# Optimization experiments

Measured on AMD Instinct MI355X. Metric: run time of the kernel, lower is better.

The kernel has to match this reference:

```python
import jax, jax.numpy as jnp
import numpy as np

B, T, D = 2048, 200, 64
H1, H2 = 80, 40
CONST_MIN = -4294967295.0


def setup_inputs() -> dict:
    key = jax.random.key(0)
    ks = jax.random.split(key, 10)
    q = jax.random.normal(ks[0], (B, D), dtype=jnp.float32)
    k = jax.random.normal(ks[1], (B, T, D), dtype=jnp.float32)
    v = jax.random.normal(ks[2], (B, T, D), dtype=jnp.float32)
    mask = jax.random.randint(ks[3], (B, T), 0, 2, dtype=jnp.int32)
    # MLP params: Dense(80, sigmoid) -> Dense(40, sigmoid) -> Dense(1)
    s1 = 1.0 / np.sqrt(4 * D)
    W1 = jax.random.normal(ks[4], (4 * D, H1), dtype=jnp.float32) * s1
    b1 = jnp.zeros((H1,), dtype=jnp.float32)
    W2 = jax.random.normal(ks[5], (H1, H2), dtype=jnp.float32) * (1.0 / np.sqrt(H1))
    b2 = jnp.zeros((H2,), dtype=jnp.float32)
    Wf = jax.random.normal(ks[6], (H2, 1), dtype=jnp.float32) * (1.0 / np.sqrt(H2))
    bf = jnp.zeros((1,), dtype=jnp.float32)
    return {"q": q, "k": k, "v": v, "mask": mask,
            "W1": W1, "b1": b1, "W2": W2, "b2": b2, "Wf": Wf, "bf": bf}


def reference(q, k, v, mask, W1, b1, W2, b2, Wf, bf):
    # q: [B,D] tiled over T -> [B,T,D]
    qt = jnp.broadcast_to(q[:, None, :], k.shape)
    # per-pair features [B,T,4D]
    info = jnp.concatenate([qt, k, qt - k, qt * k], axis=-1)
    h = jax.nn.sigmoid(jnp.einsum('btf,fh->bth', info, W1) + b1)
    h = jax.nn.sigmoid(jnp.einsum('bth,hg->btg', h, W2) + b2)
    logits = (jnp.einsum('btg,go->bto', h, Wf) + bf)[..., 0]  # [B,T]
    logits = jnp.where(mask == 0, jnp.float32(CONST_MIN), logits)
    w = jax.nn.softmax(logits, axis=-1)  # [B,T]
    out = jnp.einsum('bt,btd->bd', w, v)  # weighted sum of v
    return out
```

## Files before the change

kernel.cpp:

```cpp
#include <hip/hip_runtime.h>
#include <math.h>

#define T_LEN 200

typedef short bf8 __attribute__((ext_vector_type(8)));
typedef float f32x4 __attribute__((ext_vector_type(4)));

__device__ __forceinline__ float sigmoidf_(float x){ return 1.0f/(1.0f+__expf(-x)); }
__device__ __forceinline__ unsigned int pk_bf16(float lo, float hi){
  unsigned int r; asm("v_cvt_pk_bf16_f32 %0, %1, %2":"=v"(r):"v"(lo),"v"(hi)); return r;
}
__device__ __forceinline__ float bfu(short s){
  union{unsigned u; float f;} c; c.u = ((unsigned)(unsigned short)s)<<16; return c.f;
}
union U4B8 { uint4 u; bf8 b; };
__device__ __forceinline__ bf8 pack8(float4 x, float4 y){
  U4B8 r;
  r.u.x = pk_bf16(x.x,x.y); r.u.y = pk_bf16(x.z,x.w);
  r.u.z = pk_bf16(y.x,y.y); r.u.w = pk_bf16(y.z,y.w);
  return r.b;
}
__device__ __forceinline__ bf8 combine8(bf8 fbc, bf8 fd, float4 ql, float4 qh){
  U4B8 r;
  r.u.x = pk_bf16(fmaf(ql.x, bfu(fd[0]), bfu(fbc[0])), fmaf(ql.y, bfu(fd[1]), bfu(fbc[1])));
  r.u.y = pk_bf16(fmaf(ql.z, bfu(fd[2]), bfu(fbc[2])), fmaf(ql.w, bfu(fd[3]), bfu(fbc[3])));
  r.u.z = pk_bf16(fmaf(qh.x, bfu(fd[4]), bfu(fbc[4])), fmaf(qh.y, bfu(fd[5]), bfu(fbc[5])));
  r.u.w = pk_bf16(fmaf(qh.z, bfu(fd[6]), bfu(fbc[6])), fmaf(qh.w, bfu(fd[7]), bfu(fbc[7])));
  return r.b;
}

__global__ void prep_kernel(const float* __restrict__ W1, const float* __restrict__ W2,
                            const float* __restrict__ b2, const float* __restrict__ Wf,
                            float* __restrict__ wsf){
  unsigned short* fb = (unsigned short*)wsf;
  int i = blockIdx.x*256 + threadIdx.x;
  if (i < 15360){
    int fi = i >> 9;
    int lane = (i>>3)&63, e = i&7;
    int ht = fi/6, ks = fi%6;
    int h = ht*16 + (lane&15);
    int f = ks*32 + ((lane>>4)<<3) + e;
    float val;
    if (f < 64)        val = W1[(64+f)*80+h] - W1[(128+f)*80+h];
    else if (f < 128)  val = W1[(128+f)*80+h];
    else               val = W1[(f-128)*80+h] + W1[f*80+h];
    fb[i] = (unsigned short)(pk_bf16(val,val) & 0xffffu);
  }
  if (i < 4608){
    int fi = i >> 9;
    int lane = (i>>3)&63, e = i&7;
    int gt = fi/3, ks = fi%3;
    int g = gt*16 + (lane&15);
    int h = ks*32 + ((lane>>4)<<3) + e;
    float val;
    if (g < 40 && h < 80)       val = W2[h*40+g];
    else if (g < 40 && h == 80) val = b2[g];
    else                        val = 0.f;
    fb[15360+i] = (unsigned short)(pk_bf16(val,val) & 0xffffu);
  }
  if (i < 48){
    wsf[10032 + i] = (i<40) ? Wf[i] : 0.f;
  }
}

__global__ __launch_bounds__(64, 1) void fused_kernel(
    const float* __restrict__ q, const float* __restrict__ k, const float* __restrict__ v,
    const int* __restrict__ mask, const float* __restrict__ b1,
    const float* __restrict__ bf, const float* __restrict__ wsf,
    float* __restrict__ out)
{
  __shared__ unsigned short tl[224];
  __shared__ __align__(16) unsigned int Hw[2][16*52];
  __shared__ float e_lds[16];
  __shared__ __align__(16) unsigned int w2s[9*64*4];

  const int lane = threadIdx.x;
  const int lg = lane>>4, lc = lane&15;
  const long b = blockIdx.x;

  const float* kb = k + b*(T_LEN*64);
  const float* vb = v + b*(T_LEN*64);
  const int*   mb = mask + b*T_LEN;
  const float* qb = q + b*64;
  const unsigned short* fbg = (const unsigned short*)wsf;
  const bf8* A1f = (const bf8*)fbg;
  const uint4* A2u = (const uint4*)(fbg + 15360);
  const float* wfp = wsf + 10032;

  { uint4 z = {0,0,0,0};
    if (!(lane&1)) z.x = 0x00003F80u;
    *(uint4*)(&Hw[lane>>5][((lane&31)>>1)*52 + 40 + (lane&1)*4]) = z; }

  #pragma unroll
  for (int i=0;i<9;++i) ((uint4*)w2s)[i*64+lane] = A2u[i*64+lane];

  float4 qA0 = *(const float4*)(qb + lg*8);
  float4 qA1 = *(const float4*)(qb + lg*8 + 4);
  float4 qB0 = *(const float4*)(qb + 32 + lg*8);
  float4 qB1 = *(const float4*)(qb + 32 + lg*8 + 4);

  bf8 wk[10];
  #pragma unroll
  for (int ht=0; ht<5; ++ht){
    wk[ht*2+0] = combine8(A1f[(ht*6+0)*64+lane], A1f[(ht*6+2)*64+lane], qA0, qA1);
    wk[ht*2+1] = combine8(A1f[(ht*6+1)*64+lane], A1f[(ht*6+3)*64+lane], qB0, qB1);
  }
  float wfv[12];
  #pragma unroll
  for (int gt=0; gt<3; ++gt){
    float4 wv = *(const float4*)(wfp + gt*16 + lg*4);
    wfv[gt*4+0]=wv.x; wfv[gt*4+1]=wv.y; wfv[gt*4+2]=wv.z; wfv[gt*4+3]=wv.w;
  }

  f32x4 qacc[5];
  {
    bf8 fq0 = pack8(qA0,qA1);
    bf8 fq1 = pack8(qB0,qB1);
    #pragma unroll
    for (int ht=0; ht<5; ++ht){
      float4 bv = *(const float4*)(b1 + ht*16 + lg*4);
      qacc[ht][0]=bv.x; qacc[ht][1]=bv.y; qacc[ht][2]=bv.z; qacc[ht][3]=bv.w;
      qacc[ht] = __builtin_amdgcn_mfma_f32_16x16x32_bf16(A1f[(ht*6+4)*64+lane], fq0, qacc[ht],0,0,0);
      qacc[ht] = __builtin_amdgcn_mfma_f32_16x16x32_bf16(A1f[(ht*6+5)*64+lane], fq1, qacc[ht],0,0,0);
    }
  }
  const float bf0 = bf[0];

  int tot = 0;
  unsigned long long ltm = (1ull<<lane) - 1ull;
  #pragma unroll
  for (int c=0;c<4;++c){
    int t = c*64 + lane;
    bool f = (t < T_LEN) && (mb[t] != 0);
    unsigned long long bal = __ballot(f);
    if (f) tl[tot + (int)__popcll(bal & ltm)] = (unsigned short)t;
    tot += (int)__popcll(bal);
  }

  if (tot == 0){
    float accv = 0.f;
    for (int t=0; t<T_LEN; ++t) accv += vb[t*64 + lane];
    out[b*64 + lane] = accv * (1.0f/(float)T_LEN);
    return;
  }

  int tp = tl[min(lc, tot-1)];
  const float* kr = kb + tp*64 + lg*8;
  float4 na0 = *(const float4*)(kr);
  float4 na1 = *(const float4*)(kr+4);
  float4 nb0 = *(const float4*)(kr+32);
  float4 nb1 = *(const float4*)(kr+36);
  float vcur[16];
  #pragma unroll
  for (int i=0;i<16;++i){
    int ti = tl[min(i, tot-1)];
    vcur[i] = vb[ti*64 + lane];
  }

  float acc_pv0 = 0.f, acc_pv1 = 0.f;
  float se0 = 0.f, se1 = 0.f;
  int buf = 0;
  for (int base = 0; base < tot; base += 16, buf ^= 1){
    const bool have_next = (base + 16 < tot);
    bf8 f0 = pack8(na0,na1);
    bf8 f1 = pack8(nb0,nb1);
    float vnxt[16];
    if (have_next){
      int tn = tl[min(base+16+lc, tot-1)];
      const float* krn = kb + tn*64 + lg*8;
      na0 = *(const float4*)(krn);
      na1 = *(const float4*)(krn+4);
      nb0 = *(const float4*)(krn+32);
      nb1 = *(const float4*)(krn+36);
      #pragma unroll
      for (int i=0;i<16;++i){
        int ti = tl[min(base+16+i, tot-1)];
        vnxt[i] = vb[ti*64 + lane];
      }
    }

    f32x4 acc[5];
    #pragma unroll
    for (int ht=0; ht<5; ++ht) acc[ht] = qacc[ht];
    #pragma unroll
    for (int ht=0; ht<5; ++ht){
      acc[ht] = __builtin_amdgcn_mfma_f32_16x16x32_bf16(wk[ht*2+0], f0, acc[ht],0,0,0);
      acc[ht] = __builtin_amdgcn_mfma_f32_16x16x32_bf16(wk[ht*2+1], f1, acc[ht],0,0,0);
    }

    unsigned int* Hb = &Hw[buf][0];
    #pragma unroll
    for (int ht=0; ht<5; ++ht){
      #pragma unroll
      for (int rp=0; rp<2; ++rp)
        Hb[lc*52 + ht*8+lg*2+rp] = pk_bf16(sigmoidf_(acc[ht][2*rp]), sigmoidf_(acc[ht][2*rp+1]));
    }

    bf8 c0[3];
    #pragma unroll
    for (int ks=0; ks<3; ++ks) c0[ks] = *(const bf8*)(Hb + lc*52 + 16*ks + 4*lg);
    f32x4 g0[3];
    #pragma unroll
    for (int gt=0; gt<3; ++gt){ g0[gt][0]=0.f; g0[gt][1]=0.f; g0[gt][2]=0.f; g0[gt][3]=0.f; }
    #pragma unroll
    for (int gt=0; gt<3; ++gt){
      #pragma unroll
      for (int ks=0; ks<3; ++ks){
        bf8 wf2 = *(const bf8*)(w2s + ((gt*3+ks)*64+lane)*4);
        g0[gt] = __builtin_amdgcn_mfma_f32_16x16x32_bf16(wf2, c0[ks], g0[gt],0,0,0);
      }
    }
    float p0=0.f;
    #pragma unroll
    for (int gt=0; gt<3; ++gt){
      #pragma unroll
      for (int r=0;r<4;++r) p0 = fmaf(wfv[gt*4+r], sigmoidf_(g0[gt][r]), p0);
    }
    p0 += __shfl_xor(p0,16); p0 += __shfl_xor(p0,32);
    if (lg == 0) e_lds[lc] = (base+lc < tot) ? __expf(p0 + bf0) : 0.f;

    #pragma unroll
    for (int i=0;i<16;i+=2){
      float ei0 = e_lds[i];
      float ei1 = e_lds[i+1];
      se0 += ei0; se1 += ei1;
      acc_pv0 = fmaf(ei0, vcur[i],   acc_pv0);
      acc_pv1 = fmaf(ei1, vcur[i+1], acc_pv1);
    }
    if (have_next){
      #pragma unroll
      for (int i=0;i<16;++i) vcur[i] = vnxt[i];
    }
  }

  out[b*64 + lane] = (acc_pv0 + acc_pv1) / (se0 + se1);
}

extern "C" void kernel_launch(void* const* d_in, const int* in_sizes, int n_in,
                              void* d_out, int out_size, void* d_ws, size_t ws_size,
                              hipStream_t stream) {
  const float* q    = (const float*)d_in[0];
  const float* k    = (const float*)d_in[1];
  const float* v    = (const float*)d_in[2];
  const int*   mask = (const int*)d_in[3];
  const float* W1   = (const float*)d_in[4];
  const float* b1   = (const float*)d_in[5];
  const float* W2   = (const float*)d_in[6];
  const float* b2   = (const float*)d_in[7];
  const float* Wf   = (const float*)d_in[8];
  const float* bf   = (const float*)d_in[9];
  float* out = (float*)d_out;
  float* wsf = (float*)d_ws;

  hipLaunchKernelGGL(prep_kernel, dim3(60), dim3(256), 0, stream, W1, W2, b2, Wf, wsf);
  hipLaunchKernelGGL(fused_kernel, dim3(2048), dim3(64), 0, stream,
                     q, k, v, mask, b1, bf, wsf, out);
}
```

Measured before the change: 38.54 us.

## Process 32 keys per iteration with two interleaved MFMA chains

Widens the main loop from 16 to 32 unmasked positions per iteration. Two independent MFMA accumulator sets now interleave for both MLP layers, which adds instruction-level parallelism and halves the loop trips and barrier-like LDS round trips. The k prefetch is doubled, but v is now loaded at the top of each iteration instead of being prefetched a chunk ahead, so v load latency may be exposed. Register pressure also rises, and the single Hw buffer drops the previous double buffering.

```diff
diff --git a/kernel.cpp b/kernel.cpp
--- a/kernel.cpp
+++ b/kernel.cpp
@@ -70,8 +70,8 @@
     float* __restrict__ out)
 {
   __shared__ unsigned short tl[224];
-  __shared__ __align__(16) unsigned int Hw[2][16*52];
-  __shared__ float e_lds[16];
+  __shared__ __align__(16) unsigned int Hw[32*52];
+  __shared__ float e_lds[32];
   __shared__ __align__(16) unsigned int w2s[9*64*4];
 
   const int lane = threadIdx.x;
@@ -89,7 +89,7 @@
 
   { uint4 z = {0,0,0,0};
     if (!(lane&1)) z.x = 0x00003F80u;
-    *(uint4*)(&Hw[lane>>5][((lane&31)>>1)*52 + 40 + (lane&1)*4]) = z; }
+    *(uint4*)(&Hw[(lane>>1)*52 + 40 + (lane&1)*4]) = z; }
 
   #pragma unroll
   for (int i=0;i<9;++i) ((uint4*)w2s)[i*64+lane] = A2u[i*64+lane];
@@ -144,92 +144,112 @@
     return;
   }
 
-  int tp = tl[min(lc, tot-1)];
-  const float* kr = kb + tp*64 + lg*8;
-  float4 na0 = *(const float4*)(kr);
-  float4 na1 = *(const float4*)(kr+4);
-  float4 nb0 = *(const float4*)(kr+32);
-  float4 nb1 = *(const float4*)(kr+36);
-  float vcur[16];
-  #pragma unroll
-  for (int i=0;i<16;++i){
-    int ti = tl[min(i, tot-1)];
-    vcur[i] = vb[ti*64 + lane];
-  }
+  int t0 = tl[min(lc, tot-1)];
+  int t1 = tl[min(16+lc, tot-1)];
+  const float* kr0 = kb + t0*64 + lg*8;
+  const float* kr1 = kb + t1*64 + lg*8;
+  float4 ka0 = *(const float4*)(kr0);
+  float4 ka1 = *(const float4*)(kr0+4);
+  float4 kb0 = *(const float4*)(kr0+32);
+  float4 kb1 = *(const float4*)(kr0+36);
+  float4 kc0 = *(const float4*)(kr1);
+  float4 kc1 = *(const float4*)(kr1+4);
+  float4 kd0 = *(const float4*)(kr1+32);
+  float4 kd1 = *(const float4*)(kr1+36);
 
   float acc_pv0 = 0.f, acc_pv1 = 0.f;
   float se0 = 0.f, se1 = 0.f;
-  int buf = 0;
-  for (int base = 0; base < tot; base += 16, buf ^= 1){
-    const bool have_next = (base + 16 < tot);
-    bf8 f0 = pack8(na0,na1);
-    bf8 f1 = pack8(nb0,nb1);
-    float vnxt[16];
+  for (int base = 0; base < tot; base += 32){
+    const bool have_next = (base + 32 < tot);
+    bf8 f0 = pack8(ka0,ka1);
+    bf8 f1 = pack8(kb0,kb1);
+    bf8 f2 = pack8(kc0,kc1);
+    bf8 f3 = pack8(kd0,kd1);
+    float vcur[32];
+    #pragma unroll
+    for (int i=0;i<32;++i){
+      int ti = tl[min(base+i, tot-1)];
+      vcur[i] = vb[ti*64 + lane];
+    }
     if (have_next){
-      int tn = tl[min(base+16+lc, tot-1)];
-      const float* krn = kb + tn*64 + lg*8;
-      na0 = *(const float4*)(krn);
-      na1 = *(const float4*)(krn+4);
-      nb0 = *(const float4*)(krn+32);
-      nb1 = *(const float4*)(krn+36);
-      #pragma unroll
-      for (int i=0;i<16;++i){
-        int ti = tl[min(base+16+i, tot-1)];
-        vnxt[i] = vb[ti*64 + lane];
-      }
-    }
-
-    f32x4 acc[5];
-    #pragma unroll
-    for (int ht=0; ht<5; ++ht) acc[ht] = qacc[ht];
+      int tn0 = tl[min(base+32+lc, tot-1)];
+      int tn1 = tl[min(base+48+lc, tot-1)];
+      const float* krn0 = kb + tn0*64 + lg*8;
+      const float* krn1 = kb + tn1*64 + lg*8;
+      ka0 = *(const float4*)(krn0);
+      ka1 = *(const float4*)(krn0+4);
+      kb0 = *(const float4*)(krn0+32);
+      kb1 = *(const float4*)(krn0+36);
+      kc0 = *(const float4*)(krn1);
+      kc1 = *(const float4*)(krn1+4);
+      kd0 = *(const float4*)(krn1+32);
+      kd1 = *(const float4*)(krn1+36);
+    }
+
+    f32x4 acc0[5], acc1[5];
+    #pragma unroll
+    for (int ht=0; ht<5; ++ht){ acc0[ht] = qacc[ht]; acc1[ht] = qacc[ht]; }
     #pragma unroll
     for (int ht=0; ht<5; ++ht){
-      acc[ht] = __builtin_amdgcn_mfma_f32_16x16x32_bf16(wk[ht*2+0], f0, acc[ht],0,0,0);
-      acc[ht] = __builtin_amdgcn_mfma_f32_16x16x32_bf16(wk[ht*2+1], f1, acc[ht],0,0,0);
-    }
-
-    unsigned int* Hb = &Hw[buf][0];
+      acc0[ht] = __builtin_amdgcn_mfma_f32_16x16x32_bf16(wk[ht*2+0], f0, acc0[ht],0,0,0);
+      acc0[ht] = __builtin_amdgcn_mfma_f32_16x16x32_bf16(wk[ht*2+1], f1, acc0[ht],0,0,0);
+      acc1[ht] = __builtin_amdgcn_mfma_f32_16x16x32_bf16(wk[ht*2+0], f2, acc1[ht],0,0,0);
+      acc1[ht] = __builtin_amdgcn_mfma_f32_16x16x32_bf16(wk[ht*2+1], f3, acc1[ht],0,0,0);
+    }
+
     #pragma unroll
     for (int ht=0; ht<5; ++ht){
       #pragma unroll
-      for (int rp=0; rp<2; ++rp)
-        Hb[lc*52 + ht*8+lg*2+rp] = pk_bf16(sigmoidf_(acc[ht][2*rp]), sigmoidf_(acc[ht][2*rp+1]));
-    }
-
-    bf8 c0[3];
-    #pragma unroll
-    for (int ks=0; ks<3; ++ks) c0[ks] = *(const bf8*)(Hb + lc*52 + 16*ks + 4*lg);
-    f32x4 g0[3];
-    #pragma unroll
-    for (int gt=0; gt<3; ++gt){ g0[gt][0]=0.f; g0[gt][1]=0.f; g0[gt][2]=0.f; g0[gt][3]=0.f; }
+      for (int rp=0; rp<2; ++rp){
+        Hw[lc*52      + ht*8+lg*2+rp] = pk_bf16(sigmoidf_(acc0[ht][2*rp]), sigmoidf_(acc0[ht][2*rp+1]));
+        Hw[(16+lc)*52 + ht*8+lg*2+rp] = pk_bf16(sigmoidf_(acc1[ht][2*rp]), sigmoidf_(acc1[ht][2*rp+1]));
+      }
+    }
+
+    bf8 c0[3], c1[3];
+    #pragma unroll
+    for (int ks=0; ks<3; ++ks){
+      c0[ks] = *(const bf8*)(Hw + lc*52      + 16*ks + 4*lg);
+      c1[ks] = *(const bf8*)(Hw + (16+lc)*52 + 16*ks + 4*lg);
+    }
+    f32x4 g0[3], g1[3];
+    #pragma unroll
+    for (int gt=0; gt<3; ++gt){
+      g0[gt][0]=0.f; g0[gt][1]=0.f; g0[gt][2]=0.f; g0[gt][3]=0.f;
+      g1[gt][0]=0.f; g1[gt][1]=0.f; g1[gt][2]=0.f; g1[gt][3]=0.f;
+    }
     #pragma unroll
     for (int gt=0; gt<3; ++gt){
       #pragma unroll
       for (int ks=0; ks<3; ++ks){
         bf8 wf2 = *(const bf8*)(w2s + ((gt*3+ks)*64+lane)*4);
         g0[gt] = __builtin_amdgcn_mfma_f32_16x16x32_bf16(wf2, c0[ks], g0[gt],0,0,0);
+        g1[gt] = __builtin_amdgcn_mfma_f32_16x16x32_bf16(wf2, c1[ks], g1[gt],0,0,0);
       }
     }
-    float p0=0.f;
+    float p0=0.f, p1=0.f;
     #pragma unroll
     for (int gt=0; gt<3; ++gt){
       #pragma unroll
-      for (int r=0;r<4;++r) p0 = fmaf(wfv[gt*4+r], sigmoidf_(g0[gt][r]), p0);
+      for (int r=0;r<4;++r){
+        p0 = fmaf(wfv[gt*4+r], sigmoidf_(g0[gt][r]), p0);
+        p1 = fmaf(wfv[gt*4+r], sigmoidf_(g1[gt][r]), p1);
+      }
     }
     p0 += __shfl_xor(p0,16); p0 += __shfl_xor(p0,32);
-    if (lg == 0) e_lds[lc] = (base+lc < tot) ? __expf(p0 + bf0) : 0.f;
-
-    #pragma unroll
-    for (int i=0;i<16;i+=2){
+    p1 += __shfl_xor(p1,16); p1 += __shfl_xor(p1,32);
+    if (lg == 0){
+      e_lds[lc]    = (base+lc    < tot) ? __expf(p0 + bf0) : 0.f;
+      e_lds[16+lc] = (base+16+lc < tot) ? __expf(p1 + bf0) : 0.f;
+    }
+
+    #pragma unroll
+    for (int i=0;i<32;i+=2){
       float ei0 = e_lds[i];
       float ei1 = e_lds[i+1];
       se0 += ei0; se1 += ei1;
       acc_pv0 = fmaf(ei0, vcur[i],   acc_pv0);
       acc_pv1 = fmaf(ei1, vcur[i+1], acc_pv1);
-    }
-    if (have_next){
-      #pragma unroll
-      for (int i=0;i<16;++i) vcur[i] = vnxt[i];
     }
   }
 
```

Measured after the change: 41.32 us. +7.2%, slower.

## Pack four batch rows per 256-thread block with shared W2 staging

Applied to the files above, without the earlier changes.

The kernel now launches 512 blocks of four wavefronts, each wave handling one batch row, so the W2 fragment staging in shared memory is loaded once and shared by four waves. It also drops the register double-buffered V prefetch, loading V at the start of each chunk instead, and uses a single H buffer per wave. It adds s_setprio around the MFMA sections so waves interleave better. The aim is to raise occupancy and cut per-block setup, at the cost of a __syncthreads and less software prefetching of V.

```diff
diff --git a/kernel.cpp b/kernel.cpp
--- a/kernel.cpp
+++ b/kernel.cpp
@@ -63,20 +63,22 @@
   }
 }
 
-__global__ __launch_bounds__(64, 1) void fused_kernel(
+__global__ __launch_bounds__(256, 1) void fused_kernel(
     const float* __restrict__ q, const float* __restrict__ k, const float* __restrict__ v,
     const int* __restrict__ mask, const float* __restrict__ b1,
     const float* __restrict__ bf, const float* __restrict__ wsf,
     float* __restrict__ out)
 {
-  __shared__ unsigned short tl[224];
-  __shared__ __align__(16) unsigned int Hw[2][16*52];
-  __shared__ float e_lds[16];
+  __shared__ unsigned short tl_all[4][224];
+  __shared__ __align__(16) unsigned int Hw_all[4][16*52];
+  __shared__ float e_all[4][16];
   __shared__ __align__(16) unsigned int w2s[9*64*4];
 
-  const int lane = threadIdx.x;
+  const int tid  = threadIdx.x;
+  const int lane = tid & 63;
+  const int wid  = tid >> 6;
   const int lg = lane>>4, lc = lane&15;
-  const long b = blockIdx.x;
+  const long b = (long)blockIdx.x*4 + wid;
 
   const float* kb = k + b*(T_LEN*64);
   const float* vb = v + b*(T_LEN*64);
@@ -87,12 +89,18 @@
   const uint4* A2u = (const uint4*)(fbg + 15360);
   const float* wfp = wsf + 10032;
 
-  { uint4 z = {0,0,0,0};
+  unsigned short* tl = tl_all[wid];
+  unsigned int*   Hw = Hw_all[wid];
+  float*          e_lds = e_all[wid];
+
+  for (int j = tid; j < 576; j += 256) ((uint4*)w2s)[j] = A2u[j];
+
+  if (lane < 32){
+    uint4 z = {0,0,0,0};
     if (!(lane&1)) z.x = 0x00003F80u;
-    *(uint4*)(&Hw[lane>>5][((lane&31)>>1)*52 + 40 + (lane&1)*4]) = z; }
-
-  #pragma unroll
-  for (int i=0;i<9;++i) ((uint4*)w2s)[i*64+lane] = A2u[i*64+lane];
+    *(uint4*)(&Hw[(lane>>1)*52 + 40 + (lane&1)*4]) = z;
+  }
+  __syncthreads();
 
   float4 qA0 = *(const float4*)(qb + lg*8);
   float4 qA1 = *(const float4*)(qb + lg*8 + 4);
@@ -150,21 +158,19 @@
   float4 na1 = *(const float4*)(kr+4);
   float4 nb0 = *(const float4*)(kr+32);
   float4 nb1 = *(const float4*)(kr+36);
-  float vcur[16];
-  #pragma unroll
-  for (int i=0;i<16;++i){
-    int ti = tl[min(i, tot-1)];
-    vcur[i] = vb[ti*64 + lane];
-  }
 
   float acc_pv0 = 0.f, acc_pv1 = 0.f;
   float se0 = 0.f, se1 = 0.f;
-  int buf = 0;
-  for (int base = 0; base < tot; base += 16, buf ^= 1){
+  for (int base = 0; base < tot; base += 16){
     const bool have_next = (base + 16 < tot);
+    float vcur[16];
+    #pragma unroll
+    for (int i=0;i<16;++i){
+      int ti = tl[min(base+i, tot-1)];
+      vcur[i] = vb[ti*64 + lane];
+    }
     bf8 f0 = pack8(na0,na1);
     bf8 f1 = pack8(nb0,nb1);
-    float vnxt[16];
     if (have_next){
       int tn = tl[min(base+16+lc, tot-1)];
       const float* krn = kb + tn*64 + lg*8;
@@ -172,36 +178,33 @@
       na1 = *(const float4*)(krn+4);
       nb0 = *(const float4*)(krn+32);
       nb1 = *(const float4*)(krn+36);
-      #pragma unroll
-      for (int i=0;i<16;++i){
-        int ti = tl[min(base+16+i, tot-1)];
-        vnxt[i] = vb[ti*64 + lane];
-      }
     }
 
     f32x4 acc[5];
     #pragma unroll
     for (int ht=0; ht<5; ++ht) acc[ht] = qacc[ht];
+    __builtin_amdgcn_s_setprio(1);
     #pragma unroll
     for (int ht=0; ht<5; ++ht){
       acc[ht] = __builtin_amdgcn_mfma_f32_16x16x32_bf16(wk[ht*2+0], f0, acc[ht],0,0,0);
       acc[ht] = __builtin_amdgcn_mfma_f32_16x16x32_bf16(wk[ht*2+1], f1, acc[ht],0,0,0);
     }
-
-    unsigned int* Hb = &Hw[buf][0];
+    __builtin_amdgcn_s_setprio(0);
+
     #pragma unroll
     for (int ht=0; ht<5; ++ht){
       #pragma unroll
       for (int rp=0; rp<2; ++rp)
-        Hb[lc*52 + ht*8+lg*2+rp] = pk_bf16(sigmoidf_(acc[ht][2*rp]), sigmoidf_(acc[ht][2*rp+1]));
+        Hw[lc*52 + ht*8+lg*2+rp] = pk_bf16(sigmoidf_(acc[ht][2*rp]), sigmoidf_(acc[ht][2*rp+1]));
     }
 
     bf8 c0[3];
     #pragma unroll
-    for (int ks=0; ks<3; ++ks) c0[ks] = *(const bf8*)(Hb + lc*52 + 16*ks + 4*lg);
+    for (int ks=0; ks<3; ++ks) c0[ks] = *(const bf8*)(Hw + lc*52 + 16*ks + 4*lg);
     f32x4 g0[3];
     #pragma unroll
     for (int gt=0; gt<3; ++gt){ g0[gt][0]=0.f; g0[gt][1]=0.f; g0[gt][2]=0.f; g0[gt][3]=0.f; }
+    __builtin_amdgcn_s_setprio(1);
     #pragma unroll
     for (int gt=0; gt<3; ++gt){
       #pragma unroll
@@ -210,6 +213,7 @@
         g0[gt] = __builtin_amdgcn_mfma_f32_16x16x32_bf16(wf2, c0[ks], g0[gt],0,0,0);
       }
     }
+    __builtin_amdgcn_s_setprio(0);
     float p0=0.f;
     #pragma unroll
     for (int gt=0; gt<3; ++gt){
@@ -226,10 +230,6 @@
       se0 += ei0; se1 += ei1;
       acc_pv0 = fmaf(ei0, vcur[i],   acc_pv0);
       acc_pv1 = fmaf(ei1, vcur[i+1], acc_pv1);
-    }
-    if (have_next){
-      #pragma unroll
-      for (int i=0;i<16;++i) vcur[i] = vnxt[i];
     }
   }
 
@@ -253,6 +253,6 @@
   float* wsf = (float*)d_ws;
 
   hipLaunchKernelGGL(prep_kernel, dim3(60), dim3(256), 0, stream, W1, W2, b2, Wf, wsf);
-  hipLaunchKernelGGL(fused_kernel, dim3(2048), dim3(64), 0, stream,
+  hipLaunchKernelGGL(fused_kernel, dim3(512), dim3(256), 0, stream,
                      q, k, v, mask, b1, bf, wsf, out);
 }
```

Measured after the change: 38.28 us (median of 2 runs). No clear change (-0.7%).
